# Kernel tuning notes

Measured on AMD Instinct MI355X. Metric: run time of the kernel, lower is better.

## Reference

```python
import jax, jax.numpy as jnp
import numpy as np
import math

N_HEAD = 16

def setup_inputs() -> dict:
    key = jax.random.key(0)
    k1, k2, k3 = jax.random.split(key, 3)
    B, T, C = 4, 2048, 1024
    x = jax.random.normal(k1, (B, T, C), dtype=jnp.float32)
    W_attn = jax.random.normal(k2, (C, 3 * C), dtype=jnp.float32) * 0.02
    b_attn = jnp.zeros((3 * C,), dtype=jnp.float32)
    W_proj = jax.random.normal(k3, (C, C), dtype=jnp.float32) * 0.02
    b_proj = jnp.zeros((C,), dtype=jnp.float32)
    return {"x": x, "W_attn": W_attn, "b_attn": b_attn, "W_proj": W_proj, "b_proj": b_proj}

def reference(x, W_attn, b_attn, W_proj, b_proj):
    B, T, C = x.shape
    H = N_HEAD
    hd = C // H
    qkv = x @ W_attn + b_attn                      # [B,T,3C]
    # Faithful to source bug: q, k, v ALL built from the k-slice of qkv.
    k_slice = qkv[:, :, C:2 * C]
    k = k_slice.reshape(B, T, H, hd).transpose(0, 2, 1, 3)  # [B,H,T,hd]
    q = k
    v = k
    att = jnp.einsum('bhqd,bhkd->bhqk', q, k) / math.sqrt(hd)  # [B,H,T,T]
    causal = jnp.tril(jnp.ones((T, T), dtype=bool))
    att = jnp.where(causal[None, None], att, jnp.finfo(att.dtype).min)
    att = jax.nn.softmax(att, axis=-1)
    y = jnp.einsum('bhqk,bhkd->bhqd', att, v)      # [B,H,T,hd]
    y = y.transpose(0, 2, 1, 3).reshape(B, T, C)
    return y @ W_proj + b_proj
```

## Files before the change

kernel.cpp:

```cpp
#include <hip/hip_runtime.h>

#define T_SEQ 2048
#define C_DIM 1024
#define HD 64

typedef __attribute__((ext_vector_type(8))) short short8;
typedef __attribute__((ext_vector_type(4))) float f32x4;
typedef __attribute__((ext_vector_type(4))) unsigned int uint4v;

extern "C" __device__ float __ocml_native_exp2_f32(float);

__device__ __forceinline__ unsigned short f2bf(float f) {
  unsigned int u = __builtin_bit_cast(unsigned int, f);
  u += 0x7fffu + ((u >> 16) & 1u);
  return (unsigned short)(u >> 16);
}

__device__ __forceinline__ unsigned cvt_pk_bf16(float lo, float hi) {
  unsigned r;
  asm("v_cvt_pk_bf16_f32 %0, %1, %2" : "=v"(r) : "v"(lo), "v"(hi));
  return r;
}

__device__ __forceinline__ void gload_lds16(const void* g, void* l) {
  __builtin_amdgcn_global_load_lds(
      (const __attribute__((address_space(1))) void*)g,
      (__attribute__((address_space(3))) void*)l, 16, 0, 0);
}

__global__ __launch_bounds__(256) void prep(
    const float* __restrict__ x, unsigned short* __restrict__ xb,
    const float* __restrict__ W_attn, unsigned short* __restrict__ Wkt,
    const float* __restrict__ W_proj, unsigned short* __restrict__ Wpt) {
  int b = blockIdx.x;
  if (b < 4096) {
    size_t idx = ((size_t)b * 256 + threadIdx.x) * 8;
    const f32x4* p = (const f32x4*)(x + idx);
    f32x4 a = p[0], c = p[1];
    short8 s;
#pragma unroll
    for (int i = 0; i < 4; ++i) {
      s[i]     = (short)f2bf(a[i]);
      s[i + 4] = (short)f2bf(c[i]);
    }
    *(short8*)(xb + idx) = s;
  } else {
    __shared__ float tile[16][17];
    int b2 = b - 4096;
    const float* src;
    unsigned short* dst;
    int src_ld, col_off;
    if (b2 < 4096) { src = W_attn; dst = Wkt; src_ld = 3072; col_off = 1024; }
    else { b2 -= 4096; src = W_proj; dst = Wpt; src_ld = 1024; col_off = 0; }
    const int tx = threadIdx.x & 15, ty = threadIdx.x >> 4;
    const int bx = b2 & 63, by = b2 >> 6;
    int n = bx * 16 + tx;
    int k = by * 16 + ty;
    tile[ty][tx] = src[(size_t)k * src_ld + col_off + n];
    __syncthreads();
    int nn = bx * 16 + ty;
    int kk = by * 16 + tx;
    dst[(size_t)nn * C_DIM + kk] = f2bf(tile[tx][ty]);
  }
}

__global__ __launch_bounds__(256) void gemm_xw(
    const unsigned short* __restrict__ A, const unsigned short* __restrict__ Bt,
    const float* __restrict__ bias, unsigned short* __restrict__ out,
    unsigned short* __restrict__ vt) {
  __shared__ unsigned short Als[128 * 32];
  __shared__ unsigned short Bls[128 * 32];
  const int tid = threadIdx.x;
  const int l = tid & 63, w = tid >> 6;
  const int wr = w >> 1, wc = w & 1;
  const int rb = blockIdx.x * 128, cb = blockIdx.y * 128;
  const int brow = tid >> 2, bhalf = (tid & 3) * 8;
  f32x4 acc[4][4] = {};
  for (int kb = 0; kb < 1024; kb += 32) {
    gload_lds16(A + (size_t)(rb + brow) * 1024 + kb + bhalf,
                &Als[(size_t)w * 512]);
    gload_lds16(A + (size_t)(rb + 64 + brow) * 1024 + kb + bhalf,
                &Als[2048 + (size_t)w * 512]);
    gload_lds16(Bt + (size_t)(cb + brow) * 1024 + kb + bhalf,
                &Bls[(size_t)w * 512]);
    gload_lds16(Bt + (size_t)(cb + 64 + brow) * 1024 + kb + bhalf,
                &Bls[2048 + (size_t)w * 512]);
    __syncthreads();
    short8 af[4], bfr[4];
#pragma unroll
    for (int m = 0; m < 4; ++m)
      af[m] = *(const short8*)&Als[(wr * 64 + m * 16 + (l & 15)) * 32 + (l >> 4) * 8];
#pragma unroll
    for (int n = 0; n < 4; ++n)
      bfr[n] = *(const short8*)&Bls[(wc * 64 + n * 16 + (l & 15)) * 32 + (l >> 4) * 8];
#pragma unroll
    for (int m = 0; m < 4; ++m)
#pragma unroll
      for (int n = 0; n < 4; ++n)
        acc[m][n] = __builtin_amdgcn_mfma_f32_16x16x32_bf16(af[m], bfr[n], acc[m][n], 0, 0, 0);
    __syncthreads();
  }
  const int rg = (l >> 4) * 4, cg = l & 15;
#pragma unroll
  for (int m = 0; m < 4; ++m)
#pragma unroll
    for (int n = 0; n < 4; ++n) {
      int col = cb + wc * 64 + n * 16 + cg;
      float bv = bias[col];
      int row0 = rb + wr * 64 + m * 16 + rg;
      unsigned short e0 = f2bf(acc[m][n][0] + bv);
      unsigned short e1 = f2bf(acc[m][n][1] + bv);
      unsigned short e2 = f2bf(acc[m][n][2] + bv);
      unsigned short e3 = f2bf(acc[m][n][3] + bv);
      size_t bhd = (size_t)((row0 >> 11) * 16 + (col >> 6));
      size_t kidx = (bhd * T_SEQ + (row0 & 2047)) * HD + (col & 63);
      out[kidx]          = e0;
      out[kidx + HD]     = e1;
      out[kidx + 2 * HD] = e2;
      out[kidx + 3 * HD] = e3;
      unsigned long long pv = (unsigned long long)e0 | ((unsigned long long)e1 << 16)
                            | ((unsigned long long)e2 << 32) | ((unsigned long long)e3 << 48);
      *(unsigned long long*)&vt[(bhd * HD + (col & 63)) * T_SEQ + (row0 & 2047)] = pv;
    }
}

__global__ __launch_bounds__(256) void gemm_yw(
    const unsigned short* __restrict__ A, const unsigned short* __restrict__ Bt,
    const float* __restrict__ bias, float* __restrict__ out) {
  __shared__ unsigned short Als[128 * 32];
  __shared__ unsigned short Bls[128 * 32];
  const int tid = threadIdx.x;
  const int l = tid & 63, w = tid >> 6;
  const int wr = w >> 1, wc = w & 1;
  const int rb = blockIdx.x * 128, cb = blockIdx.y * 128;
  const int brow = tid >> 2, bhalf = (tid & 3) * 8;
  f32x4 acc[4][4] = {};
  for (int kb = 0; kb < 1024; kb += 32) {
    gload_lds16(A + (size_t)(rb + brow) * 1024 + kb + bhalf,
                &Als[(size_t)w * 512]);
    gload_lds16(A + (size_t)(rb + 64 + brow) * 1024 + kb + bhalf,
                &Als[2048 + (size_t)w * 512]);
    gload_lds16(Bt + (size_t)(cb + brow) * 1024 + kb + bhalf,
                &Bls[(size_t)w * 512]);
    gload_lds16(Bt + (size_t)(cb + 64 + brow) * 1024 + kb + bhalf,
                &Bls[2048 + (size_t)w * 512]);
    __syncthreads();
    short8 af[4], bfr[4];
#pragma unroll
    for (int m = 0; m < 4; ++m)
      af[m] = *(const short8*)&Als[(wr * 64 + m * 16 + (l & 15)) * 32 + (l >> 4) * 8];
#pragma unroll
    for (int n = 0; n < 4; ++n)
      bfr[n] = *(const short8*)&Bls[(wc * 64 + n * 16 + (l & 15)) * 32 + (l >> 4) * 8];
#pragma unroll
    for (int m = 0; m < 4; ++m)
#pragma unroll
      for (int n = 0; n < 4; ++n)
        acc[m][n] = __builtin_amdgcn_mfma_f32_16x16x32_bf16(af[m], bfr[n], acc[m][n], 0, 0, 0);
    __syncthreads();
  }
  const int rg = (l >> 4) * 4, cg = l & 15;
#pragma unroll
  for (int m = 0; m < 4; ++m)
#pragma unroll
    for (int n = 0; n < 4; ++n) {
      int col = cb + wc * 64 + n * 16 + cg;
      float bv = bias[col];
#pragma unroll
      for (int r = 0; r < 4; ++r) {
        int row = rb + wr * 64 + m * 16 + rg + r;
        out[(size_t)row * 1024 + col] = acc[m][n][r] + bv;
      }
    }
}

__device__ __forceinline__ void sm_group(
    f32x4 (&s)[4], int qq, int kvb, bool needmask, int g,
    float& mrun, float& lrun, f32x4 (&yacc)[4],
    int src01, int src23, bool hi2, short8 (&pa)[2]) {
  if (needmask) {
    const int lim = qq - kvb;
#pragma unroll
    for (int b = 0; b < 4; ++b)
#pragma unroll
      for (int r = 0; r < 4; ++r)
        if (16 * b + 4 * g + r > lim) s[b][r] = -INFINITY;
  }
  float mt = fmaxf(fmaxf(s[0][0], s[0][1]), fmaxf(s[0][2], s[0][3]));
#pragma unroll
  for (int b = 1; b < 4; ++b)
    mt = fmaxf(mt, fmaxf(fmaxf(s[b][0], s[b][1]), fmaxf(s[b][2], s[b][3])));
  mt = fmaxf(mt, __shfl_xor(mt, 16));
  mt = fmaxf(mt, __shfl_xor(mt, 32));
  if (!__all(mt <= mrun + 11.5416f)) {
    float mn = fmaxf(mrun, mt);
    float al = __ocml_native_exp2_f32(mrun - mn);
    mrun = mn;
    lrun *= al;
    float a0 = __shfl(al, 4 * g + 0);
    float a1 = __shfl(al, 4 * g + 1);
    float a2 = __shfl(al, 4 * g + 2);
    float a3 = __shfl(al, 4 * g + 3);
#pragma unroll
    for (int nb = 0; nb < 4; ++nb) {
      yacc[nb][0] *= a0; yacc[nb][1] *= a1;
      yacc[nb][2] *= a2; yacc[nb][3] *= a3;
    }
  }
  float ps = 0.f;
  unsigned pk[4][2];
#pragma unroll
  for (int b = 0; b < 4; ++b) {
    float p0 = __ocml_native_exp2_f32(s[b][0] - mrun);
    float p1 = __ocml_native_exp2_f32(s[b][1] - mrun);
    float p2 = __ocml_native_exp2_f32(s[b][2] - mrun);
    float p3 = __ocml_native_exp2_f32(s[b][3] - mrun);
    ps += (p0 + p1) + (p2 + p3);
    pk[b][0] = cvt_pk_bf16(p0, p1);
    pk[b][1] = cvt_pk_bf16(p2, p3);
  }
  ps += __shfl_xor(ps, 16);
  ps += __shfl_xor(ps, 32);
  lrun += ps;
  {
    unsigned x0a = (unsigned)__shfl((int)pk[0][0], src01);
    unsigned x1a = (unsigned)__shfl((int)pk[1][0], src01);
    unsigned x0b = (unsigned)__shfl((int)pk[0][1], src01);
    unsigned x1b = (unsigned)__shfl((int)pk[1][1], src01);
    unsigned y0a = (unsigned)__shfl((int)pk[0][0], src23);
    unsigned y1a = (unsigned)__shfl((int)pk[1][0], src23);
    unsigned y0b = (unsigned)__shfl((int)pk[0][1], src23);
    unsigned y1b = (unsigned)__shfl((int)pk[1][1], src23);
    uint4v u;
    u.x = hi2 ? x1a : x0a;
    u.y = hi2 ? x1b : x0b;
    u.z = hi2 ? y1a : y0a;
    u.w = hi2 ? y1b : y0b;
    pa[0] = __builtin_bit_cast(short8, u);
  }
  {
    unsigned x0a = (unsigned)__shfl((int)pk[2][0], src01);
    unsigned x1a = (unsigned)__shfl((int)pk[3][0], src01);
    unsigned x0b = (unsigned)__shfl((int)pk[2][1], src01);
    unsigned x1b = (unsigned)__shfl((int)pk[3][1], src01);
    unsigned y0a = (unsigned)__shfl((int)pk[2][0], src23);
    unsigned y1a = (unsigned)__shfl((int)pk[3][0], src23);
    unsigned y0b = (unsigned)__shfl((int)pk[2][1], src23);
    unsigned y1b = (unsigned)__shfl((int)pk[3][1], src23);
    uint4v u;
    u.x = hi2 ? x1a : x0a;
    u.y = hi2 ? x1b : x0b;
    u.z = hi2 ? y1a : y0a;
    u.w = hi2 ? y1b : y0b;
    pa[1] = __builtin_bit_cast(short8, u);
  }
}

__global__ __launch_bounds__(128, 4) void attn_fwd(
    const unsigned short* __restrict__ Khb, const unsigned short* __restrict__ Vt,
    unsigned short* __restrict__ Y) {
  const int id = blockIdx.x;
  const int xcd = id & 7;
  const int r8  = id >> 3;
  const int bh  = xcd * 8 + (r8 & 7);
  const int chunk = 63 - (r8 >> 3);
  const int tid = threadIdx.x;
  const int w = tid >> 6;
  const int l = tid & 63;
  const int i = l & 15, g = l >> 4;
  const unsigned short* kbase = Khb + (size_t)bh * T_SEQ * HD;
  const unsigned short* vbase = Vt + (size_t)bh * HD * T_SEQ;

  const int q0 = chunk * 32;
  const int qA = q0 + i, qB = q0 + 16 + i;
  const int nt = (q0 + 31) / 64 + 1;
  const int half = (nt + 1) >> 1;
  const int tBeg = w ? half : 0;
  const int tEnd = w ? nt : half;

  __shared__ float Ylds[32][68];
  __shared__ float Mlds[32];
  __shared__ float Llds[32];

  short8 qa0 = *(const short8*)(kbase + (size_t)qA * HD + g * 8);
  short8 qa1 = *(const short8*)(kbase + (size_t)qA * HD + 32 + g * 8);
  short8 qb0 = *(const short8*)(kbase + (size_t)qB * HD + g * 8);
  short8 qb1 = *(const short8*)(kbase + (size_t)qB * HD + 32 + g * 8);

  f32x4 ya[4] = {}, yb[4] = {};
  float mA = -INFINITY, lA = 0.f, mB = -INFINITY, lB = 0.f;

  const int src01 = i + ((g & 1) << 5);
  const int src23 = src01 + 16;
  const bool hi2 = (g >> 1) != 0;
  const float SCL = 0.18033688f;

#pragma unroll 2
  for (int t = tBeg; t < tEnd; ++t) {
    const int kvb = t * 64;
    f32x4 sa[4], sb[4];
#pragma unroll
    for (int b = 0; b < 4; ++b) {
      const unsigned short* kp = kbase + (size_t)(kvb + 16 * b + i) * HD + g * 8;
      short8 k0 = *(const short8*)kp;
      short8 k1 = *(const short8*)(kp + 32);
      f32x4 acc = {};
      acc = __builtin_amdgcn_mfma_f32_16x16x32_bf16(k0, qa0, acc, 0, 0, 0);
      acc = __builtin_amdgcn_mfma_f32_16x16x32_bf16(k1, qa1, acc, 0, 0, 0);
      sa[b] = acc;
      f32x4 acc2 = {};
      acc2 = __builtin_amdgcn_mfma_f32_16x16x32_bf16(k0, qb0, acc2, 0, 0, 0);
      acc2 = __builtin_amdgcn_mfma_f32_16x16x32_bf16(k1, qb1, acc2, 0, 0, 0);
      sb[b] = acc2;
    }
#pragma unroll
    for (int b = 0; b < 4; ++b)
#pragma unroll
      for (int r = 0; r < 4; ++r) { sa[b][r] *= SCL; sb[b][r] *= SCL; }

    const bool needmask = (kvb + 63 > q0);
    short8 paA[2], paB[2];
    sm_group(sa, qA, kvb, needmask, g, mA, lA, ya, src01, src23, hi2, paA);
    sm_group(sb, qB, kvb, needmask, g, mB, lB, yb, src01, src23, hi2, paB);

#pragma unroll
    for (int c = 0; c < 2; ++c)
#pragma unroll
      for (int nb = 0; nb < 4; ++nb) {
        short8 vf = *(const short8*)(vbase + (size_t)(nb * 16 + i) * T_SEQ + kvb + c * 32 + g * 8);
        ya[nb] = __builtin_amdgcn_mfma_f32_16x16x32_bf16(paA[c], vf, ya[nb], 0, 0, 0);
        yb[nb] = __builtin_amdgcn_mfma_f32_16x16x32_bf16(paB[c], vf, yb[nb], 0, 0, 0);
      }
  }

  if (w == 1) {
#pragma unroll
    for (int nb = 0; nb < 4; ++nb)
#pragma unroll
      for (int r = 0; r < 4; ++r) {
        Ylds[4 * g + r][nb * 16 + i]      = ya[nb][r];
        Ylds[16 + 4 * g + r][nb * 16 + i] = yb[nb][r];
      }
    if (l < 16) {
      Mlds[l]      = mA;
      Llds[l]      = lA;
      Mlds[16 + l] = mB;
      Llds[16 + l] = lB;
    }
  }
  __syncthreads();
  if (w == 0) {
    const int bb = bh >> 4, hh = bh & 15;
    size_t rowA = ((size_t)bb * T_SEQ + q0 + 4 * g) * C_DIM;
#pragma unroll
    for (int r = 0; r < 4; ++r) {
      float m0 = __shfl(mA, 4 * g + r);
      float l0 = __shfl(lA, 4 * g + r);
      float m1 = Mlds[4 * g + r];
      float l1 = Llds[4 * g + r];
      float mm = fmaxf(m0, m1);
      float e0 = __ocml_native_exp2_f32(m0 - mm);
      float e1 = __ocml_native_exp2_f32(m1 - mm);
      float inv = 1.f / (l0 * e0 + l1 * e1);
      float w0 = e0 * inv, w1 = e1 * inv;
#pragma unroll
      for (int nb = 0; nb < 4; ++nb) {
        int col = hh * 64 + nb * 16 + i;
        Y[rowA + (size_t)r * C_DIM + col] =
            f2bf(ya[nb][r] * w0 + Ylds[4 * g + r][nb * 16 + i] * w1);
      }
    }
    size_t rowB = rowA + (size_t)16 * C_DIM;
#pragma unroll
    for (int r = 0; r < 4; ++r) {
      float m0 = __shfl(mB, 4 * g + r);
      float l0 = __shfl(lB, 4 * g + r);
      float m1 = Mlds[16 + 4 * g + r];
      float l1 = Llds[16 + 4 * g + r];
      float mm = fmaxf(m0, m1);
      float e0 = __ocml_native_exp2_f32(m0 - mm);
      float e1 = __ocml_native_exp2_f32(m1 - mm);
      float inv = 1.f / (l0 * e0 + l1 * e1);
      float w0 = e0 * inv, w1 = e1 * inv;
#pragma unroll
      for (int nb = 0; nb < 4; ++nb) {
        int col = hh * 64 + nb * 16 + i;
        Y[rowB + (size_t)r * C_DIM + col] =
            f2bf(yb[nb][r] * w0 + Ylds[16 + 4 * g + r][nb * 16 + i] * w1);
      }
    }
  }
}

extern "C" void kernel_launch(void* const* d_in, const int* in_sizes, int n_in,
                              void* d_out, int out_size, void* d_ws, size_t ws_size,
                              hipStream_t stream) {
  const float* x      = (const float*)d_in[0];
  const float* W_attn = (const float*)d_in[1];
  const float* b_attn = (const float*)d_in[2];
  const float* W_proj = (const float*)d_in[3];
  const float* b_proj = (const float*)d_in[4];
  float* out = (float*)d_out;

  unsigned short* Wkt  = (unsigned short*)d_ws;
  unsigned short* Wpt  = Wkt + (size_t)1024 * 1024;
  unsigned short* Khb  = Wpt + (size_t)1024 * 1024;
  unsigned short* Ybuf = Khb + (size_t)8192 * 1024;
  unsigned short* Vtb  = Ybuf + (size_t)8192 * 1024;
  unsigned short* xb   = Ybuf;

  prep<<<dim3(12288), 256, 0, stream>>>(x, xb, W_attn, Wkt, W_proj, Wpt);

  gemm_xw<<<dim3(64, 8), 256, 0, stream>>>(xb, Wkt, b_attn + 1024, Khb, Vtb);

  attn_fwd<<<dim3(4096), 128, 0, stream>>>(Khb, Vtb, Ybuf);

  gemm_yw<<<dim3(64, 8), 256, 0, stream>>>(Ybuf, Wpt, b_proj, out);
}
```

Measured before the change: 197.7 us.

## Double-buffer LDS tiles in both projection GEMMs to overlap loads with MFMA

Both GEMM kernels (QKV projection and output projection) now keep two LDS buffers per operand. Each iteration prefetches the next K-slice into the spare buffer while the current slice is consumed by MFMA, which also removes one barrier per iteration. The aim is to hide global-to-LDS load latency behind compute. In exchange, LDS use per block doubles, which may lower occupancy, and correctness relies on the barrier waiting for the asynchronous LDS loads to finish.

```diff
diff --git a/kernel.cpp b/kernel.cpp
--- a/kernel.cpp
+++ b/kernel.cpp
@@ -68,38 +68,48 @@
     const unsigned short* __restrict__ A, const unsigned short* __restrict__ Bt,
     const float* __restrict__ bias, unsigned short* __restrict__ out,
     unsigned short* __restrict__ vt) {
-  __shared__ unsigned short Als[128 * 32];
-  __shared__ unsigned short Bls[128 * 32];
+  __shared__ unsigned short Als[2][128 * 32];
+  __shared__ unsigned short Bls[2][128 * 32];
   const int tid = threadIdx.x;
   const int l = tid & 63, w = tid >> 6;
   const int wr = w >> 1, wc = w & 1;
   const int rb = blockIdx.x * 128, cb = blockIdx.y * 128;
   const int brow = tid >> 2, bhalf = (tid & 3) * 8;
   f32x4 acc[4][4] = {};
+
+#define STAGE_XW(BUF, KB)                                                     \
+  do {                                                                        \
+    gload_lds16(A + (size_t)(rb + brow) * 1024 + (KB) + bhalf,                \
+                &Als[BUF][(size_t)w * 512]);                                  \
+    gload_lds16(A + (size_t)(rb + 64 + brow) * 1024 + (KB) + bhalf,           \
+                &Als[BUF][2048 + (size_t)w * 512]);                           \
+    gload_lds16(Bt + (size_t)(cb + brow) * 1024 + (KB) + bhalf,               \
+                &Bls[BUF][(size_t)w * 512]);                                  \
+    gload_lds16(Bt + (size_t)(cb + 64 + brow) * 1024 + (KB) + bhalf,          \
+                &Bls[BUF][2048 + (size_t)w * 512]);                           \
+  } while (0)
+
+  STAGE_XW(0, 0);
+  int cur = 0;
   for (int kb = 0; kb < 1024; kb += 32) {
-    gload_lds16(A + (size_t)(rb + brow) * 1024 + kb + bhalf,
-                &Als[(size_t)w * 512]);
-    gload_lds16(A + (size_t)(rb + 64 + brow) * 1024 + kb + bhalf,
-                &Als[2048 + (size_t)w * 512]);
-    gload_lds16(Bt + (size_t)(cb + brow) * 1024 + kb + bhalf,
-                &Bls[(size_t)w * 512]);
-    gload_lds16(Bt + (size_t)(cb + 64 + brow) * 1024 + kb + bhalf,
-                &Bls[2048 + (size_t)w * 512]);
     __syncthreads();
+    if (kb + 32 < 1024) STAGE_XW(cur ^ 1, kb + 32);
     short8 af[4], bfr[4];
 #pragma unroll
     for (int m = 0; m < 4; ++m)
-      af[m] = *(const short8*)&Als[(wr * 64 + m * 16 + (l & 15)) * 32 + (l >> 4) * 8];
+      af[m] = *(const short8*)&Als[cur][(wr * 64 + m * 16 + (l & 15)) * 32 + (l >> 4) * 8];
 #pragma unroll
     for (int n = 0; n < 4; ++n)
-      bfr[n] = *(const short8*)&Bls[(wc * 64 + n * 16 + (l & 15)) * 32 + (l >> 4) * 8];
+      bfr[n] = *(const short8*)&Bls[cur][(wc * 64 + n * 16 + (l & 15)) * 32 + (l >> 4) * 8];
 #pragma unroll
     for (int m = 0; m < 4; ++m)
 #pragma unroll
       for (int n = 0; n < 4; ++n)
         acc[m][n] = __builtin_amdgcn_mfma_f32_16x16x32_bf16(af[m], bfr[n], acc[m][n], 0, 0, 0);
-    __syncthreads();
-  }
+    cur ^= 1;
+  }
+#undef STAGE_XW
+
   const int rg = (l >> 4) * 4, cg = l & 15;
 #pragma unroll
   for (int m = 0; m < 4; ++m)
@@ -127,38 +137,48 @@
 __global__ __launch_bounds__(256) void gemm_yw(
     const unsigned short* __restrict__ A, const unsigned short* __restrict__ Bt,
     const float* __restrict__ bias, float* __restrict__ out) {
-  __shared__ unsigned short Als[128 * 32];
-  __shared__ unsigned short Bls[128 * 32];
+  __shared__ unsigned short Als[2][128 * 32];
+  __shared__ unsigned short Bls[2][128 * 32];
   const int tid = threadIdx.x;
   const int l = tid & 63, w = tid >> 6;
   const int wr = w >> 1, wc = w & 1;
   const int rb = blockIdx.x * 128, cb = blockIdx.y * 128;
   const int brow = tid >> 2, bhalf = (tid & 3) * 8;
   f32x4 acc[4][4] = {};
+
+#define STAGE_YW(BUF, KB)                                                     \
+  do {                                                                        \
+    gload_lds16(A + (size_t)(rb + brow) * 1024 + (KB) + bhalf,                \
+                &Als[BUF][(size_t)w * 512]);                                  \
+    gload_lds16(A + (size_t)(rb + 64 + brow) * 1024 + (KB) + bhalf,           \
+                &Als[BUF][2048 + (size_t)w * 512]);                           \
+    gload_lds16(Bt + (size_t)(cb + brow) * 1024 + (KB) + bhalf,               \
+                &Bls[BUF][(size_t)w * 512]);                                  \
+    gload_lds16(Bt + (size_t)(cb + 64 + brow) * 1024 + (KB) + bhalf,          \
+                &Bls[BUF][2048 + (size_t)w * 512]);                           \
+  } while (0)
+
+  STAGE_YW(0, 0);
+  int cur = 0;
   for (int kb = 0; kb < 1024; kb += 32) {
-    gload_lds16(A + (size_t)(rb + brow) * 1024 + kb + bhalf,
-                &Als[(size_t)w * 512]);
-    gload_lds16(A + (size_t)(rb + 64 + brow) * 1024 + kb + bhalf,
-                &Als[2048 + (size_t)w * 512]);
-    gload_lds16(Bt + (size_t)(cb + brow) * 1024 + kb + bhalf,
-                &Bls[(size_t)w * 512]);
-    gload_lds16(Bt + (size_t)(cb + 64 + brow) * 1024 + kb + bhalf,
-                &Bls[2048 + (size_t)w * 512]);
     __syncthreads();
+    if (kb + 32 < 1024) STAGE_YW(cur ^ 1, kb + 32);
     short8 af[4], bfr[4];
 #pragma unroll
     for (int m = 0; m < 4; ++m)
-      af[m] = *(const short8*)&Als[(wr * 64 + m * 16 + (l & 15)) * 32 + (l >> 4) * 8];
+      af[m] = *(const short8*)&Als[cur][(wr * 64 + m * 16 + (l & 15)) * 32 + (l >> 4) * 8];
 #pragma unroll
     for (int n = 0; n < 4; ++n)
-      bfr[n] = *(const short8*)&Bls[(wc * 64 + n * 16 + (l & 15)) * 32 + (l >> 4) * 8];
+      bfr[n] = *(const short8*)&Bls[cur][(wc * 64 + n * 16 + (l & 15)) * 32 + (l >> 4) * 8];
 #pragma unroll
     for (int m = 0; m < 4; ++m)
 #pragma unroll
       for (int n = 0; n < 4; ++n)
         acc[m][n] = __builtin_amdgcn_mfma_f32_16x16x32_bf16(af[m], bfr[n], acc[m][n], 0, 0, 0);
-    __syncthreads();
-  }
+    cur ^= 1;
+  }
+#undef STAGE_YW
+
   const int rg = (l >> 4) * 4, cg = l & 15;
 #pragma unroll
   for (int m = 0; m < 4; ++m)
```

After: 193.0 us (median of 3 runs). 2.4% less time.
